# Kernel optimization log

Hardware: AMD Instinct MI355X
Metric: run time of the kernel (lower is better)

The kernel has to match this reference:

```python
import jax, jax.numpy as jnp
import numpy as np
import math

KERNEL_SIZES = [3, 5, 7, 7, 9, 9]
DILATIONS = [1, 2, 1, 3, 1, 2]
NUM_HEADS = 6
HEAD_DIM = 32  # in_channels 192 / 6 heads


def _neighborhood_patches(t, k, dil):
    """Equivalent of F.unfold(t, kernel_size=k, dilation=dil, padding=dil*(k//2)).
    t: [B, d, H, W] -> [B, d, k*k, H, W] (zero-padded borders, torch unfold ordering:
    patch index p = i*k + j over the kernel window, row-major)."""
    B, d, H, W = t.shape
    pad = dil * (k // 2)
    tp = jnp.pad(t, ((0, 0), (0, 0), (pad, pad), (pad, pad)))
    pats = [tp[:, :, i * dil:i * dil + H, j * dil:j * dil + W]
            for i in range(k) for j in range(k)]
    return jnp.stack(pats, axis=2)


def setup_inputs() -> dict:
    key = jax.random.key(0)
    ks = jax.random.split(key, 3 + NUM_HEADS)
    B, C, H, W = 4, 192, 96, 96
    x = jax.random.normal(ks[0], (B, C, H, W), dtype=jnp.float32)
    w_qkv = jax.random.normal(ks[1], (3 * C, C), dtype=jnp.float32) * 0.02  # 1x1 conv weight
    w_out = jax.random.normal(ks[2], (C, C), dtype=jnp.float32) * 0.02      # 1x1 conv weight
    inp = {"x": x, "w_qkv": w_qkv, "w_out": w_out}
    for i, k in enumerate(KERNEL_SIZES):
        # module inits biases to zeros; use small randn so softmax path is exercised
        inp[f"b{i}"] = jax.random.normal(ks[3 + i], (k * k,), dtype=jnp.float32) * 0.02
    return inp


def reference(x, w_qkv, w_out, b0, b1, b2, b3, b4, b5):
    biases = [b0, b1, b2, b3, b4, b5]
    B, C, H, W = x.shape
    scale = 1.0 / math.sqrt(HEAD_DIM)
    # 1x1 conv qkv projection
    qkv = jnp.einsum('bchw,oc->bohw', x, w_qkv)
    q, k, v = jnp.split(qkv, 3, axis=1)
    q = q.reshape(B, NUM_HEADS, HEAD_DIM, H, W)
    k = k.reshape(B, NUM_HEADS, HEAD_DIM, H, W)
    v = v.reshape(B, NUM_HEADS, HEAD_DIM, H, W)
    head_outs = []
    for i in range(NUM_HEADS):  # heads have structurally different (k, dilation)
        ksz, dil = KERNEL_SIZES[i], DILATIONS[i]
        kp = _neighborhood_patches(k[:, i], ksz, dil)  # [B, d, k*k, H, W]
        vp = _neighborhood_patches(v[:, i], ksz, dil)  # [B, d, k*k, H, W]
        scores = jnp.einsum('bdhw,bdphw->bphw', q[:, i], kp) * scale
        scores = scores + biases[i][None, :, None, None]
        attn = jax.nn.softmax(scores, axis=1)  # softmax over the k*k neighborhood
        head_outs.append(jnp.einsum('bphw,bdphw->bdhw', attn, vp))
    out = jnp.concatenate(head_outs, axis=1)  # [B, C, H, W]
    return jnp.einsum('bchw,oc->bohw', out, w_out)
```

## Files before the change

kernel.cpp:

```cpp
#include <hip/hip_runtime.h>
#include <hip/hip_bf16.h>
#include <math.h>

#define NPIX 9216
#define HDIM 96
#define WDIM 96
#define NHEADS 6
#define BATCH 4

typedef __bf16 bf16x8 __attribute__((ext_vector_type(8)));
typedef float  f32x4  __attribute__((ext_vector_type(4)));

struct Bias6 { const float* p[6]; };

__device__ __forceinline__ void cp16(void* ldst, const void* gsrc) {
    __builtin_amdgcn_global_load_lds(
        (const __attribute__((address_space(1))) unsigned int*)gsrc,
        (__attribute__((address_space(3))) unsigned int*)ldst, 16, 0, 0);
}

__device__ __forceinline__ unsigned short bfbits(__bf16 x) { return *(unsigned short*)&x; }

__device__ __forceinline__ unsigned packf16(float a, float b) {
    _Float16 ha = (_Float16)a, hb = (_Float16)b;
    return (unsigned)*(unsigned short*)&ha | ((unsigned)*(unsigned short*)&hb << 16);
}

#define MIX_LL(acc, kk, qq) asm("v_fma_mix_f32 %0, %1, %2, %0 op_sel:[0,0,0] op_sel_hi:[1,1,0]" : "+v"(acc) : "v"(kk), "v"(qq))
#define MIX_HH(acc, kk, qq) asm("v_fma_mix_f32 %0, %1, %2, %0 op_sel:[1,1,0] op_sel_hi:[1,1,0]" : "+v"(acc) : "v"(kk), "v"(qq))
#define MIX_LF(acc, vv, ee) asm("v_fma_mix_f32 %0, %1, %2, %0 op_sel:[0,0,0] op_sel_hi:[1,0,0]" : "+v"(acc) : "v"(vv), "v"(ee))
#define MIX_HF(acc, vv, ee) asm("v_fma_mix_f32 %0, %1, %2, %0 op_sel:[1,0,0] op_sel_hi:[1,0,0]" : "+v"(acc) : "v"(vv), "v"(ee))

__global__ __launch_bounds__(256) void convert_w(
    const float* __restrict__ w1, __bf16* __restrict__ h1, __bf16* __restrict__ l1, int n1,
    const float* __restrict__ w2, __bf16* __restrict__ h2, __bf16* __restrict__ l2, int n2)
{
    const int i = blockIdx.x * 256 + threadIdx.x;
    if (i < n1) { float f = w1[i]; __bf16 h = (__bf16)f; h1[i] = h; l1[i] = (__bf16)(f - (float)h); }
    if (i < n2) { float f = w2[i]; __bf16 h = (__bf16)f; h2[i] = h; l2[i] = (__bf16)(f - (float)h); }
}

__global__ __launch_bounds__(256) void convert_x(
    const float* __restrict__ x, __bf16* __restrict__ Xh)
{
    __shared__ float t[32][65];
    const int b  = blockIdx.z;
    const int c0 = blockIdx.y * 32;
    const int p0 = blockIdx.x * 64;
    const int tid = threadIdx.x;
    const int pl = tid & 63;
    #pragma unroll
    for (int i = 0; i < 8; ++i) {
        const int c = i * 4 + (tid >> 6);
        t[c][pl] = x[((size_t)b * 192 + c0 + c) * NPIX + p0 + pl];
    }
    __syncthreads();
    const int p  = tid >> 2;
    const int cq = (tid & 3) * 8;
    bf16x8 vh;
    #pragma unroll
    for (int j = 0; j < 8; ++j)
        vh[j] = (__bf16)t[cq + j][p];
    *(bf16x8*)(Xh + ((size_t)b * NPIX + p0 + p) * 192 + c0 + cq) = vh;
}

template<int MODE>
__global__ __launch_bounds__(256) void gemm_mfma(
    const __bf16* __restrict__ Ah, const __bf16* __restrict__ Al,
    const __bf16* __restrict__ Bh,
    void* __restrict__ Yv, int M)
{
    __shared__ __bf16 sAh[64 * 64];
    __shared__ __bf16 sAl[64 * 64];
    __shared__ __bf16 sBh[128 * 64];

    const int b  = blockIdx.z;
    const int n0 = blockIdx.x * 128;
    const int m0 = blockIdx.y * 64;
    const int tid  = threadIdx.x;
    const int lane = tid & 63;
    const int wid  = tid >> 6;
    const int wr = wid >> 1, wc = wid & 1;
    const int lr = lane & 15;
    const int kg = lane >> 4;

    const char* gA_h = (const char*)Ah + (size_t)m0 * 384;
    const char* gA_l = (const char*)Al + (size_t)m0 * 384;
    const char* gB   = (const char*)Bh + ((size_t)b * NPIX + n0) * 384;

    f32x4 acc[2][4];
    #pragma unroll
    for (int mf = 0; mf < 2; ++mf)
        #pragma unroll
        for (int nf = 0; nf < 4; ++nf)
            acc[mf][nf] = (f32x4){0.f, 0.f, 0.f, 0.f};

    for (int ks = 0; ks < 3; ++ks) {
        if (ks) __syncthreads();
        const int kb = ks * 128;
        #pragma unroll
        for (int it = 0; it < 2; ++it) {
            const int d  = it * 256 + tid;
            const int rd = d >> 3, cd = d & 7;
            const size_t src = (size_t)rd * 384 + kb + ((cd ^ (rd & 7)) << 4);
            cp16((char*)sAh + d * 16, gA_h + src);
            cp16((char*)sAl + d * 16, gA_l + src);
        }
        #pragma unroll
        for (int it = 0; it < 4; ++it) {
            const int d  = it * 256 + tid;
            const int rd = d >> 3, cd = d & 7;
            const size_t src = (size_t)rd * 384 + kb + ((cd ^ (rd & 7)) << 4);
            cp16((char*)sBh + d * 16, gB + src);
        }
        __syncthreads();
        #pragma unroll
        for (int s = 0; s < 2; ++s) {
            bf16x8 aH[2], aL[2], bH[4];
            #pragma unroll
            for (int mf = 0; mf < 2; ++mf) {
                const int row = wr * 32 + mf * 16 + lr;
                const int c = (s * 4 + kg) ^ (row & 7);
                aH[mf] = *(const bf16x8*)((const char*)sAh + row * 128 + c * 16);
                aL[mf] = *(const bf16x8*)((const char*)sAl + row * 128 + c * 16);
            }
            #pragma unroll
            for (int nf = 0; nf < 4; ++nf) {
                const int row = wc * 64 + nf * 16 + lr;
                const int c = (s * 4 + kg) ^ (row & 7);
                bH[nf] = *(const bf16x8*)((const char*)sBh + row * 128 + c * 16);
            }
            #pragma unroll
            for (int mf = 0; mf < 2; ++mf)
                #pragma unroll
                for (int nf = 0; nf < 4; ++nf) {
                    acc[mf][nf] = __builtin_amdgcn_mfma_f32_16x16x32_bf16(aH[mf], bH[nf], acc[mf][nf], 0, 0, 0);
                    acc[mf][nf] = __builtin_amdgcn_mfma_f32_16x16x32_bf16(aL[mf], bH[nf], acc[mf][nf], 0, 0, 0);
                }
        }
    }

    if (MODE == 0) {
        float* Yb = (float*)Yv + ((size_t)b * M + m0 + wr * 32) * NPIX + n0 + wc * 64;
        #pragma unroll
        for (int mf = 0; mf < 2; ++mf)
            #pragma unroll
            for (int r = 0; r < 4; ++r) {
                const int row = mf * 16 + kg * 4 + r;
                #pragma unroll
                for (int nf = 0; nf < 4; ++nf)
                    Yb[(size_t)row * NPIX + nf * 16 + lr] = acc[mf][nf][r];
            }
    } else {
        #pragma unroll
        for (int mf = 0; mf < 2; ++mf) {
            const int cbase = m0 + wr * 32 + mf * 16 + kg * 4;
            unsigned* Yq = (unsigned*)Yv
                + (((size_t)b * 72 + (cbase >> 3)) * NPIX + n0 + wc * 64 + lr) * 4
                + ((kg & 1) << 1);
            #pragma unroll
            for (int nf = 0; nf < 4; ++nf) {
                Yq[(nf * 16) * 4 + 0] = packf16(acc[mf][nf][0], acc[mf][nf][1]);
                Yq[(nf * 16) * 4 + 1] = packf16(acc[mf][nf][2], acc[mf][nf][3]);
            }
        }
    }
}

#define MAX_REGION 1300

template<int KSZ, int DIL>
__device__ __forceinline__ void attn_body(
    const uint4* __restrict__ Qq, const uint4* __restrict__ Kq,
    const uint4* __restrict__ Vq, const float* __restrict__ bias,
    __bf16* __restrict__ oh, int h0, int w0,
    uint4* __restrict__ lds,
    unsigned (* __restrict__ out_lds)[256])
{
    constexpr int CC  = KSZ / 2;
    constexpr int HAL = CC * DIL;
    constexpr int R   = 8 + 2 * HAL;
    constexpr int C   = 32 + 2 * HAL;
    constexpr int RC  = R * C;
    constexpr int NN  = KSZ * KSZ;
    const float scale = 0.17677669529663689f;

    const int tx = threadIdx.x & 31;
    const int ty = threadIdx.x >> 5;
    const int pix = (h0 + ty) * WDIM + (w0 + tx);
    const int lb = ty * C + tx;

    float score[NN];
    #pragma unroll
    for (int n = 0; n < NN; ++n) score[n] = 0.f;

    for (int pp = 0; pp < 4; ++pp) {
        __syncthreads();
        for (int idx = threadIdx.x; idx < RC; idx += 256) {
            const int r = idx / C, c = idx - r * C;
            const int gh = h0 - HAL + r, gw = w0 - HAL + c;
            uint4 v = make_uint4(0u, 0u, 0u, 0u);
            if ((unsigned)gh < (unsigned)HDIM && (unsigned)gw < (unsigned)WDIM)
                v = Kq[(size_t)pp * NPIX + gh * WDIM + gw];
            lds[idx] = v;
        }
        __syncthreads();
        const uint4 qv = Qq[(size_t)pp * NPIX + pix];
        #pragma unroll
        for (int i = 0; i < KSZ; ++i)
            #pragma unroll
            for (int j = 0; j < KSZ; ++j) {
                const uint4 k8 = lds[lb + i * DIL * C + j * DIL];
                float s = score[i * KSZ + j];
                MIX_LL(s, k8.x, qv.x); MIX_HH(s, k8.x, qv.x);
                MIX_LL(s, k8.y, qv.y); MIX_HH(s, k8.y, qv.y);
                MIX_LL(s, k8.z, qv.z); MIX_HH(s, k8.z, qv.z);
                MIX_LL(s, k8.w, qv.w); MIX_HH(s, k8.w, qv.w);
                score[i * KSZ + j] = s;
            }
    }

    float l = 0.f;
    #pragma unroll
    for (int n = 0; n < NN; ++n) {
        const float e = __expf(score[n] * scale + bias[n]);
        l += e;
        score[n] = e;
    }
    const float inv = 1.f / l;

    #pragma unroll
    for (int half = 0; half < 2; ++half) {
        #pragma unroll
        for (int rr = 0; rr < 2; ++rr) {
            const int pp = half * 2 + rr;
            __syncthreads();
            for (int idx = threadIdx.x; idx < RC; idx += 256) {
                const int r = idx / C, c = idx - r * C;
                const int gh = h0 - HAL + r, gw = w0 - HAL + c;
                uint4 v = make_uint4(0u, 0u, 0u, 0u);
                if ((unsigned)gh < (unsigned)HDIM && (unsigned)gw < (unsigned)WDIM)
                    v = Vq[(size_t)pp * NPIX + gh * WDIM + gw];
                lds[idx] = v;
            }
            __syncthreads();
            float a0 = 0.f, a1 = 0.f, a2 = 0.f, a3 = 0.f;
            float a4 = 0.f, a5 = 0.f, a6 = 0.f, a7 = 0.f;
            #pragma unroll
            for (int i = 0; i < KSZ; ++i)
                #pragma unroll
                for (int j = 0; j < KSZ; ++j) {
                    const uint4 v8 = lds[lb + i * DIL * C + j * DIL];
                    const float e = score[i * KSZ + j];
                    MIX_LF(a0, v8.x, e); MIX_HF(a1, v8.x, e);
                    MIX_LF(a2, v8.y, e); MIX_HF(a3, v8.y, e);
                    MIX_LF(a4, v8.z, e); MIX_HF(a5, v8.z, e);
                    MIX_LF(a6, v8.w, e); MIX_HF(a7, v8.w, e);
                }
            const __bf16 c0 = (__bf16)(a0 * inv), c1 = (__bf16)(a1 * inv);
            const __bf16 c2 = (__bf16)(a2 * inv), c3 = (__bf16)(a3 * inv);
            const __bf16 c4 = (__bf16)(a4 * inv), c5 = (__bf16)(a5 * inv);
            const __bf16 c6 = (__bf16)(a6 * inv), c7 = (__bf16)(a7 * inv);
            out_lds[rr * 4 + 0][threadIdx.x] = (unsigned)bfbits(c0) | ((unsigned)bfbits(c1) << 16);
            out_lds[rr * 4 + 1][threadIdx.x] = (unsigned)bfbits(c2) | ((unsigned)bfbits(c3) << 16);
            out_lds[rr * 4 + 2][threadIdx.x] = (unsigned)bfbits(c4) | ((unsigned)bfbits(c5) << 16);
            out_lds[rr * 4 + 3][threadIdx.x] = (unsigned)bfbits(c6) | ((unsigned)bfbits(c7) << 16);
        }
        __syncthreads();
        #pragma unroll
        for (int it = 0; it < 2; ++it) {
            const int linear = it * 256 + threadIdx.x;
            const int px = linear >> 1;
            const int c  = linear & 1;
            const int gpix = (h0 + (px >> 5)) * WDIM + w0 + (px & 31);
            uint4 val = make_uint4(out_lds[c * 4 + 0][px], out_lds[c * 4 + 1][px],
                                   out_lds[c * 4 + 2][px], out_lds[c * 4 + 3][px]);
            *((uint4*)((unsigned*)(oh + (size_t)gpix * 192)) + half * 2 + c) = val;
        }
    }
}

__global__ __launch_bounds__(256) void attn_kernel(
    const uint4* __restrict__ qkv, Bias6 bs, __bf16* __restrict__ ATh)
{
    __shared__ uint4 lds[MAX_REGION];
    __shared__ unsigned out_lds[8][256];

    const int orig = blockIdx.x;
    const int wg = (orig & 7) * 108 + (orig >> 3);
    const int panel = wg / 36;
    const int tile = wg - panel * 36;
    const int chunk = panel / 3, slot = panel - chunk * 3;
    int head, b;
    if (slot == 0)      { head = 4 + (chunk >> 2); b = chunk & 3; }
    else if (slot == 1) { head = 2 + (chunk >> 2); b = chunk & 3; }
    else                { head = (chunk < 4) ? 1 : 0; b = chunk & 3; }
    const int tx = tile % 3, ty = tile / 3;
    const int w0 = tx * 32, h0 = ty * 8;

    const uint4* base = qkv + (size_t)b * 72 * NPIX;
    const uint4* Qq = base + (size_t)(head * 4) * NPIX;
    const uint4* Kq = base + (size_t)(24 + head * 4) * NPIX;
    const uint4* Vq = base + (size_t)(48 + head * 4) * NPIX;
    __bf16* oh = ATh + (size_t)b * NPIX * 192 + head * 32;
    const float* bias = bs.p[head];

    switch (head) {
        case 0: attn_body<3, 1>(Qq, Kq, Vq, bias, oh, h0, w0, lds, out_lds); break;
        case 1: attn_body<5, 2>(Qq, Kq, Vq, bias, oh, h0, w0, lds, out_lds); break;
        case 2: attn_body<7, 1>(Qq, Kq, Vq, bias, oh, h0, w0, lds, out_lds); break;
        case 3: attn_body<7, 3>(Qq, Kq, Vq, bias, oh, h0, w0, lds, out_lds); break;
        case 4: attn_body<9, 1>(Qq, Kq, Vq, bias, oh, h0, w0, lds, out_lds); break;
        case 5: attn_body<9, 2>(Qq, Kq, Vq, bias, oh, h0, w0, lds, out_lds); break;
    }
}

extern "C" void kernel_launch(void* const* d_in, const int* in_sizes, int n_in,
                              void* d_out, int out_size, void* d_ws, size_t ws_size,
                              hipStream_t stream) {
    const float* x     = (const float*)d_in[0];
    const float* w_qkv = (const float*)d_in[1];
    const float* w_out = (const float*)d_in[2];
    Bias6 bs;
    for (int i = 0; i < 6; ++i) bs.p[i] = (const float*)d_in[3 + i];
    float* out = (float*)d_out;

    char* ws = (char*)d_ws;
    uint4* QKV = (uint4*)ws;            ws += (size_t)BATCH * 72 * NPIX * 16;
    __bf16* Xh  = (__bf16*)ws;          ws += (size_t)BATCH * NPIX * 192 * 2;
    __bf16* ATh = (__bf16*)ws;          ws += (size_t)BATCH * NPIX * 192 * 2;
    __bf16* W1h = (__bf16*)ws;          ws += (size_t)576 * 192 * 2;
    __bf16* W1l = (__bf16*)ws;          ws += (size_t)576 * 192 * 2;
    __bf16* W2h = (__bf16*)ws;          ws += (size_t)192 * 192 * 2;
    __bf16* W2l = (__bf16*)ws;          ws += (size_t)192 * 192 * 2;

    convert_w<<<dim3((576 * 192 + 255) / 256), 256, 0, stream>>>(
        w_qkv, W1h, W1l, 576 * 192, w_out, W2h, W2l, 192 * 192);
    convert_x<<<dim3(NPIX / 64, 192 / 32, BATCH), 256, 0, stream>>>(x, Xh);

    gemm_mfma<1><<<dim3(NPIX / 128, 576 / 64, BATCH), 256, 0, stream>>>(
        W1h, W1l, Xh, (void*)QKV, 576);

    attn_kernel<<<dim3(864), 256, 0, stream>>>(QKV, bs, ATh);

    gemm_mfma<0><<<dim3(NPIX / 128, 192 / 64, BATCH), 256, 0, stream>>>(
        W2h, W2l, ATh, (void*)out, 192);
}
```

Measured before the change: 97.38 us.

## Double-buffer K/V halo tiles with async global-to-LDS loads in attention

Replaces the synchronous register-staged K/V halo loads with direct global_load_lds copies, double-buffered across the 8 K/V octet rounds so the next tile loads while the current one is consumed. Out-of-bounds halo elements read from a zeroed guard buffer, which is cleared by a memset on every launch. Q vectors are preloaded into registers, and the bias is folded into the initial score so the softmax no longer adds it. The manual vmcnt waits and raw barriers add fragility, and the larger LDS footprint may reduce occupancy. The dilation-3 head keeps a single buffer.

```diff
diff --git a/kernel.cpp b/kernel.cpp
--- a/kernel.cpp
+++ b/kernel.cpp
@@ -24,6 +24,16 @@
 __device__ __forceinline__ unsigned packf16(float a, float b) {
     _Float16 ha = (_Float16)a, hb = (_Float16)b;
     return (unsigned)*(unsigned short*)&ha | ((unsigned)*(unsigned short*)&hb << 16);
+}
+
+template<int N>
+__device__ __forceinline__ void waitcnt_vm() {
+    if constexpr (N == 0) asm volatile("s_waitcnt vmcnt(0)" ::: "memory");
+    else if constexpr (N == 2) asm volatile("s_waitcnt vmcnt(2)" ::: "memory");
+    else if constexpr (N == 3) asm volatile("s_waitcnt vmcnt(3)" ::: "memory");
+    else if constexpr (N == 5) asm volatile("s_waitcnt vmcnt(5)" ::: "memory");
+    else asm volatile("s_waitcnt vmcnt(0)" ::: "memory");
+    __builtin_amdgcn_sched_barrier(0);
 }
 
 #define MIX_LL(acc, kk, qq) asm("v_fma_mix_f32 %0, %1, %2, %0 op_sel:[0,0,0] op_sel_hi:[1,1,0]" : "+v"(acc) : "v"(kk), "v"(qq))
@@ -167,14 +177,13 @@
     }
 }
 
-#define MAX_REGION 1300
-
-template<int KSZ, int DIL>
+template<int KSZ, int DIL, bool DB, int L>
 __device__ __forceinline__ void attn_body(
     const uint4* __restrict__ Qq, const uint4* __restrict__ Kq,
     const uint4* __restrict__ Vq, const float* __restrict__ bias,
+    const uint4* __restrict__ guard,
     __bf16* __restrict__ oh, int h0, int w0,
-    uint4* __restrict__ lds,
+    uint4* __restrict__ bufs,
     unsigned (* __restrict__ out_lds)[256])
 {
     constexpr int CC  = KSZ / 2;
@@ -185,91 +194,93 @@
     constexpr int NN  = KSZ * KSZ;
     const float scale = 0.17677669529663689f;
 
-    const int tx = threadIdx.x & 31;
-    const int ty = threadIdx.x >> 5;
+    const int tid = threadIdx.x;
+    const int tx = tid & 31;
+    const int ty = tid >> 5;
     const int pix = (h0 + ty) * WDIM + (w0 + tx);
     const int lb = ty * C + tx;
 
+    uint4 qv[4];
+    #pragma unroll
+    for (int p = 0; p < 4; ++p) qv[p] = Qq[(size_t)p * NPIX + pix];
+
     float score[NN];
     #pragma unroll
-    for (int n = 0; n < NN; ++n) score[n] = 0.f;
-
-    for (int pp = 0; pp < 4; ++pp) {
-        __syncthreads();
-        for (int idx = threadIdx.x; idx < RC; idx += 256) {
-            const int r = idx / C, c = idx - r * C;
-            const int gh = h0 - HAL + r, gw = w0 - HAL + c;
-            uint4 v = make_uint4(0u, 0u, 0u, 0u);
-            if ((unsigned)gh < (unsigned)HDIM && (unsigned)gw < (unsigned)WDIM)
-                v = Kq[(size_t)pp * NPIX + gh * WDIM + gw];
-            lds[idx] = v;
-        }
-        __syncthreads();
-        const uint4 qv = Qq[(size_t)pp * NPIX + pix];
+    for (int n = 0; n < NN; ++n) score[n] = bias[n] * 5.656854249492381f;
+
+    auto STAGE = [&](int r) {
+        const uint4* src = (r < 4) ? (Kq + (size_t)r * NPIX)
+                                   : (Vq + (size_t)(r - 4) * NPIX);
+        uint4* dst = bufs + (DB ? ((r & 1) * (L * 256)) : 0);
+        #pragma unroll
+        for (int it = 0; it < L; ++it) {
+            const int idx = it * 256 + tid;
+            const int rr = idx / C, cc = idx - rr * C;
+            const int gh = h0 - HAL + rr, gw = w0 - HAL + cc;
+            const bool ok = (idx < RC) && ((unsigned)gh < (unsigned)HDIM)
+                                       && ((unsigned)gw < (unsigned)WDIM);
+            const uint4* s = ok ? (src + gh * WDIM + gw) : guard;
+            cp16(dst + idx, s);
+        }
+    };
+
+    auto QK = [&](const uint4* buf, int oct) {
+        const uint4 q = qv[oct];
         #pragma unroll
         for (int i = 0; i < KSZ; ++i)
             #pragma unroll
             for (int j = 0; j < KSZ; ++j) {
-                const uint4 k8 = lds[lb + i * DIL * C + j * DIL];
+                const uint4 k8 = buf[lb + i * DIL * C + j * DIL];
                 float s = score[i * KSZ + j];
-                MIX_LL(s, k8.x, qv.x); MIX_HH(s, k8.x, qv.x);
-                MIX_LL(s, k8.y, qv.y); MIX_HH(s, k8.y, qv.y);
-                MIX_LL(s, k8.z, qv.z); MIX_HH(s, k8.z, qv.z);
-                MIX_LL(s, k8.w, qv.w); MIX_HH(s, k8.w, qv.w);
+                MIX_LL(s, k8.x, q.x); MIX_HH(s, k8.x, q.x);
+                MIX_LL(s, k8.y, q.y); MIX_HH(s, k8.y, q.y);
+                MIX_LL(s, k8.z, q.z); MIX_HH(s, k8.z, q.z);
+                MIX_LL(s, k8.w, q.w); MIX_HH(s, k8.w, q.w);
                 score[i * KSZ + j] = s;
             }
-    }
-
-    float l = 0.f;
-    #pragma unroll
-    for (int n = 0; n < NN; ++n) {
-        const float e = __expf(score[n] * scale + bias[n]);
-        l += e;
-        score[n] = e;
-    }
-    const float inv = 1.f / l;
-
-    #pragma unroll
-    for (int half = 0; half < 2; ++half) {
-        #pragma unroll
-        for (int rr = 0; rr < 2; ++rr) {
-            const int pp = half * 2 + rr;
-            __syncthreads();
-            for (int idx = threadIdx.x; idx < RC; idx += 256) {
-                const int r = idx / C, c = idx - r * C;
-                const int gh = h0 - HAL + r, gw = w0 - HAL + c;
-                uint4 v = make_uint4(0u, 0u, 0u, 0u);
-                if ((unsigned)gh < (unsigned)HDIM && (unsigned)gw < (unsigned)WDIM)
-                    v = Vq[(size_t)pp * NPIX + gh * WDIM + gw];
-                lds[idx] = v;
-            }
-            __syncthreads();
-            float a0 = 0.f, a1 = 0.f, a2 = 0.f, a3 = 0.f;
-            float a4 = 0.f, a5 = 0.f, a6 = 0.f, a7 = 0.f;
-            #pragma unroll
-            for (int i = 0; i < KSZ; ++i)
-                #pragma unroll
-                for (int j = 0; j < KSZ; ++j) {
-                    const uint4 v8 = lds[lb + i * DIL * C + j * DIL];
-                    const float e = score[i * KSZ + j];
-                    MIX_LF(a0, v8.x, e); MIX_HF(a1, v8.x, e);
-                    MIX_LF(a2, v8.y, e); MIX_HF(a3, v8.y, e);
-                    MIX_LF(a4, v8.z, e); MIX_HF(a5, v8.z, e);
-                    MIX_LF(a6, v8.w, e); MIX_HF(a7, v8.w, e);
-                }
-            const __bf16 c0 = (__bf16)(a0 * inv), c1 = (__bf16)(a1 * inv);
-            const __bf16 c2 = (__bf16)(a2 * inv), c3 = (__bf16)(a3 * inv);
-            const __bf16 c4 = (__bf16)(a4 * inv), c5 = (__bf16)(a5 * inv);
-            const __bf16 c6 = (__bf16)(a6 * inv), c7 = (__bf16)(a7 * inv);
-            out_lds[rr * 4 + 0][threadIdx.x] = (unsigned)bfbits(c0) | ((unsigned)bfbits(c1) << 16);
-            out_lds[rr * 4 + 1][threadIdx.x] = (unsigned)bfbits(c2) | ((unsigned)bfbits(c3) << 16);
-            out_lds[rr * 4 + 2][threadIdx.x] = (unsigned)bfbits(c4) | ((unsigned)bfbits(c5) << 16);
-            out_lds[rr * 4 + 3][threadIdx.x] = (unsigned)bfbits(c6) | ((unsigned)bfbits(c7) << 16);
-        }
-        __syncthreads();
+    };
+
+    float inv = 0.f;
+    auto SOFTMAX = [&]() {
+        float l = 0.f;
+        #pragma unroll
+        for (int n = 0; n < NN; ++n) {
+            const float e = __expf(score[n] * scale);
+            l += e;
+            score[n] = e;
+        }
+        inv = 1.f / l;
+    };
+
+    auto PV = [&](const uint4* buf, int oct) {
+        float a0 = 0.f, a1 = 0.f, a2 = 0.f, a3 = 0.f;
+        float a4 = 0.f, a5 = 0.f, a6 = 0.f, a7 = 0.f;
+        #pragma unroll
+        for (int i = 0; i < KSZ; ++i)
+            #pragma unroll
+            for (int j = 0; j < KSZ; ++j) {
+                const uint4 v8 = buf[lb + i * DIL * C + j * DIL];
+                const float e = score[i * KSZ + j];
+                MIX_LF(a0, v8.x, e); MIX_HF(a1, v8.x, e);
+                MIX_LF(a2, v8.y, e); MIX_HF(a3, v8.y, e);
+                MIX_LF(a4, v8.z, e); MIX_HF(a5, v8.z, e);
+                MIX_LF(a6, v8.w, e); MIX_HF(a7, v8.w, e);
+            }
+        const int rr = oct & 1;
+        const __bf16 c0 = (__bf16)(a0 * inv), c1 = (__bf16)(a1 * inv);
+        const __bf16 c2 = (__bf16)(a2 * inv), c3 = (__bf16)(a3 * inv);
+        const __bf16 c4 = (__bf16)(a4 * inv), c5 = (__bf16)(a5 * inv);
+        const __bf16 c6 = (__bf16)(a6 * inv), c7 = (__bf16)(a7 * inv);
+        out_lds[rr * 4 + 0][tid] = (unsigned)bfbits(c0) | ((unsigned)bfbits(c1) << 16);
+        out_lds[rr * 4 + 1][tid] = (unsigned)bfbits(c2) | ((unsigned)bfbits(c3) << 16);
+        out_lds[rr * 4 + 2][tid] = (unsigned)bfbits(c4) | ((unsigned)bfbits(c5) << 16);
+        out_lds[rr * 4 + 3][tid] = (unsigned)bfbits(c6) | ((unsigned)bfbits(c7) << 16);
+    };
+
+    auto COOP = [&](int half) {
         #pragma unroll
         for (int it = 0; it < 2; ++it) {
-            const int linear = it * 256 + threadIdx.x;
+            const int linear = it * 256 + tid;
             const int px = linear >> 1;
             const int c  = linear & 1;
             const int gpix = (h0 + (px >> 5)) * WDIM + w0 + (px & 31);
@@ -277,13 +288,55 @@
                                    out_lds[c * 4 + 2][px], out_lds[c * 4 + 3][px]);
             *((uint4*)((unsigned*)(oh + (size_t)gpix * 192)) + half * 2 + c) = val;
         }
+    };
+
+    if constexpr (DB) {
+        STAGE(0);
+        #pragma unroll
+        for (int r = 0; r < 8; ++r) {
+            if (r < 7) STAGE(r + 1);
+            if (r < 7) waitcnt_vm<L>(); else waitcnt_vm<0>();
+            __builtin_amdgcn_s_barrier();
+            __builtin_amdgcn_sched_barrier(0);
+            const uint4* buf = bufs + (r & 1) * (L * 256);
+            if (r < 4) {
+                QK(buf, r);
+                if (r == 3) SOFTMAX();
+            } else {
+                PV(buf, r - 4);
+                asm volatile("s_waitcnt lgkmcnt(0)" ::: "memory");
+                __builtin_amdgcn_sched_barrier(0);
+            }
+            __builtin_amdgcn_s_barrier();
+            __builtin_amdgcn_sched_barrier(0);
+            if (r == 5) COOP(0);
+            if (r == 7) COOP(1);
+        }
+    } else {
+        #pragma unroll
+        for (int r = 0; r < 8; ++r) {
+            __syncthreads();
+            if (r == 6) COOP(0);
+            STAGE(r);
+            __syncthreads();
+            const uint4* buf = bufs;
+            if (r < 4) {
+                QK(buf, r);
+                if (r == 3) SOFTMAX();
+            } else {
+                PV(buf, r - 4);
+            }
+        }
+        __syncthreads();
+        COOP(1);
     }
 }
 
 __global__ __launch_bounds__(256) void attn_kernel(
-    const uint4* __restrict__ qkv, Bias6 bs, __bf16* __restrict__ ATh)
+    const uint4* __restrict__ qkv, Bias6 bs, __bf16* __restrict__ ATh,
+    const uint4* __restrict__ guard)
 {
-    __shared__ uint4 lds[MAX_REGION];
+    __shared__ uint4 bufs[2560];
     __shared__ unsigned out_lds[8][256];
 
     const int orig = blockIdx.x;
@@ -306,12 +359,12 @@
     const float* bias = bs.p[head];
 
     switch (head) {
-        case 0: attn_body<3, 1>(Qq, Kq, Vq, bias, oh, h0, w0, lds, out_lds); break;
-        case 1: attn_body<5, 2>(Qq, Kq, Vq, bias, oh, h0, w0, lds, out_lds); break;
-        case 2: attn_body<7, 1>(Qq, Kq, Vq, bias, oh, h0, w0, lds, out_lds); break;
-        case 3: attn_body<7, 3>(Qq, Kq, Vq, bias, oh, h0, w0, lds, out_lds); break;
-        case 4: attn_body<9, 1>(Qq, Kq, Vq, bias, oh, h0, w0, lds, out_lds); break;
-        case 5: attn_body<9, 2>(Qq, Kq, Vq, bias, oh, h0, w0, lds, out_lds); break;
+        case 0: attn_body<3, 1, true, 2>(Qq, Kq, Vq, bias, guard, oh, h0, w0, bufs, out_lds); break;
+        case 1: attn_body<5, 2, true, 3>(Qq, Kq, Vq, bias, guard, oh, h0, w0, bufs, out_lds); break;
+        case 2: attn_body<7, 1, true, 3>(Qq, Kq, Vq, bias, guard, oh, h0, w0, bufs, out_lds); break;
+        case 3: attn_body<7, 3, false, 6>(Qq, Kq, Vq, bias, guard, oh, h0, w0, bufs, out_lds); break;
+        case 4: attn_body<9, 1, true, 3>(Qq, Kq, Vq, bias, guard, oh, h0, w0, bufs, out_lds); break;
+        case 5: attn_body<9, 2, true, 5>(Qq, Kq, Vq, bias, guard, oh, h0, w0, bufs, out_lds); break;
     }
 }
 
@@ -333,6 +386,9 @@
     __bf16* W1l = (__bf16*)ws;          ws += (size_t)576 * 192 * 2;
     __bf16* W2h = (__bf16*)ws;          ws += (size_t)192 * 192 * 2;
     __bf16* W2l = (__bf16*)ws;          ws += (size_t)192 * 192 * 2;
+    uint4* guard = (uint4*)ws;          ws += 1024;
+
+    hipMemsetAsync(guard, 0, 1024, stream);
 
     convert_w<<<dim3((576 * 192 + 255) / 256), 256, 0, stream>>>(
         w_qkv, W1h, W1l, 576 * 192, w_out, W2h, W2l, 192 * 192);
@@ -341,7 +397,7 @@
     gemm_mfma<1><<<dim3(NPIX / 128, 576 / 64, BATCH), 256, 0, stream>>>(
         W1h, W1l, Xh, (void*)QKV, 576);
 
-    attn_kernel<<<dim3(864), 256, 0, stream>>>(QKV, bs, ATh);
+    attn_kernel<<<dim3(864), 256, 0, stream>>>(QKV, bs, ATh, guard);
 
     gemm_mfma<0><<<dim3(NPIX / 128, 192 / 64, BATCH), 256, 0, stream>>>(
         W2h, W2l, ATh, (void*)out, 192);
```

Result: faster. 94.70 us (-2.8%).
